# Kernel optimization log

Measured on AMD Instinct MI355X. Metric: run time of the kernel, lower is better.

The kernel has to match this reference:

```python
import jax, jax.numpy as jnp
import numpy as np

NEG_SLOPE = 0.2


def gatv2_layer(x, Wl, Wr, att, bias, src, dst, n_nodes, heads, ch, concat):
    # Wl: source-side transform (lin_l), Wr: target-side transform (lin_r)
    xl = (x @ Wl).reshape(n_nodes, heads, ch)  # [N,H,C] source features
    xr = (x @ Wr).reshape(n_nodes, heads, ch)  # [N,H,C] target features
    m = xl[src] + xr[dst]                       # [E,H,C]
    e = jax.nn.leaky_relu(m, NEG_SLOPE)
    logits = jnp.einsum('ehc,hc->eh', e, att)   # [E,H]
    # segment softmax over destination nodes
    mx = jax.ops.segment_max(logits, dst, num_segments=n_nodes)  # [N,H]
    ex = jnp.exp(logits - mx[dst])
    denom = jax.ops.segment_sum(ex, dst, num_segments=n_nodes)   # [N,H]
    alpha = ex / denom[dst]                                       # [E,H]
    out = jax.ops.segment_sum(alpha[:, :, None] * xl[src], dst,
                              num_segments=n_nodes)              # [N,H,C]
    if concat:
        out = out.reshape(n_nodes, heads * ch)
    else:
        out = out.mean(axis=1)
    return out + bias


def setup_inputs() -> dict:
    N, E = 50000, 800000
    IN, HID, OUT, H = 256, 64, 256, 4
    key = jax.random.key(0)
    ks = jax.random.split(key, 12)
    s = lambda fan_in: 1.0 / np.sqrt(fan_in)
    return {
        'x': jax.random.normal(ks[0], (N, IN), dtype=jnp.float32),
        'edge_index': jax.random.randint(ks[1], (2, E), 0, N, dtype=jnp.int64),
        'Wl1': jax.random.normal(ks[2], (IN, H * HID), jnp.float32) * s(IN),
        'Wr1': jax.random.normal(ks[3], (IN, H * HID), jnp.float32) * s(IN),
        'att1': jax.random.normal(ks[4], (H, HID), jnp.float32) * s(HID),
        'b1': jnp.zeros((H * HID,), jnp.float32),
        'Wl2': jax.random.normal(ks[5], (H * HID, OUT), jnp.float32) * s(H * HID),
        'Wr2': jax.random.normal(ks[6], (H * HID, OUT), jnp.float32) * s(H * HID),
        'att2': jax.random.normal(ks[7], (1, OUT), jnp.float32) * s(OUT),
        'b2': jnp.zeros((OUT,), jnp.float32),
    }


def reference(x, edge_index, Wl1, Wr1, att1, b1, Wl2, Wr2, att2, b2):
    N = x.shape[0]
    # PyG GATv2Conv default: add self-loops
    loops = jnp.arange(N, dtype=edge_index.dtype)
    src = jnp.concatenate([edge_index[0], loops])
    dst = jnp.concatenate([edge_index[1], loops])
    # dropout(p=0.6) is identity in eval mode
    h = gatv2_layer(x, Wl1, Wr1, att1, b1, src, dst, N, 4, 64, concat=True)
    h = jax.nn.elu(h)
    out = gatv2_layer(h, Wl2, Wr2, att2, b2, src, dst, N, 1, 256, concat=False)
    return out
```

## Files before the change

kernel.cpp:

```cpp
#include <hip/hip_runtime.h>
#include <hip/hip_fp16.h>
#include <cstdint>

using u16 = unsigned short;
using f32x4 = __attribute__((ext_vector_type(4))) float;
using short8 = __attribute__((ext_vector_type(8))) short;
using half8  = __attribute__((ext_vector_type(8))) _Float16;
using bfv8   = __attribute__((ext_vector_type(8))) __bf16;

__device__ __forceinline__ float bf2f(u16 u) {
    unsigned int v = ((unsigned int)u) << 16;
    float f; __builtin_memcpy(&f, &v, 4); return f;
}
__device__ __forceinline__ u16 f2bf(float f) {
    unsigned int u; __builtin_memcpy(&u, &f, 4);
    u += 0x7fffu + ((u >> 16) & 1u);
    return (u16)(u >> 16);
}
__device__ __forceinline__ float sane(float f) {
    return (f == f && f > -1e30f && f < 1e30f) ? f : 0.f;
}
__device__ __forceinline__ float ld16(u16 v, int isf16) {
    float fb = bf2f(v);
    __half hh; __builtin_memcpy(&hh, &v, 2);
    float fh = __half2float(hh);
    return isf16 ? fh : fb;
}
__device__ __forceinline__ u16 st16(float f, int isf16) {
    __half hh = __float2half(f);
    u16 vh; __builtin_memcpy(&vh, &hh, 2);
    return isf16 ? vh : f2bf(f);
}
__device__ __forceinline__ float ldf(const void* p, size_t i, int mode) {
    if (mode == 2) return sane(((const float*)p)[i]);
    return sane(ld16(((const u16*)p)[i], mode == 1));
}
__device__ __forceinline__ void stf(void* p, size_t i, int mode, float f) {
    if (mode == 2) { ((float*)p)[i] = f; return; }
    ((u16*)p)[i] = st16(f, mode == 1);
}
template <int ISF16> __device__ __forceinline__ float dec(u16 v);
template <> __device__ __forceinline__ float dec<0>(u16 v) { return bf2f(v); }
template <> __device__ __forceinline__ float dec<1>(u16 v) {
    __half hh; __builtin_memcpy(&hh, &v, 2); return __half2float(hh);
}
template <int CTRL, int RM>
__device__ __forceinline__ float dpp_add(float v) {
    int s = __builtin_amdgcn_update_dpp(0, __builtin_bit_cast(int, v), CTRL, RM, 0xF, true);
    return v + __builtin_bit_cast(float, s);
}

__global__ void zero_k(int* __restrict__ p, int n) {
    int i = blockIdx.x * 256 + threadIdx.x;
    if (i < n) p[i] = 0;
}

__global__ void det_k(const u16* __restrict__ x, int* __restrict__ flag) {
    __shared__ int sLow, sF32;
    if (threadIdx.x == 0) { sLow = 0; sF32 = 0; }
    __syncthreads();
    int low = 0, f32 = 0;
    for (int w = threadIdx.x; w < 2048; w += 256) {
        u16 lo = x[2 * w], hi = x[2 * w + 1];
        int e_lo = (lo >> 7) & 0xFF, e_hi = (hi >> 7) & 0xFF;
        low += (e_lo < 104) + (e_hi < 104);
        unsigned int word = ((unsigned int)hi << 16) | lo;
        int e32 = (word >> 23) & 0xFF;
        f32 += (e32 >= 97 && e32 <= 157) ? 1 : 0;
    }
    atomicAdd(&sLow, low); atomicAdd(&sF32, f32);
    __syncthreads();
    if (threadIdx.x == 0) {
        int mode = 0;
        if (sLow > 327) mode = (sF32 > 1843) ? 2 : 1;
        flag[1] = mode;
    }
}

__global__ void probe_idx(const int* __restrict__ ei, int* __restrict__ flag) {
    int t = threadIdx.x;
    int v = ei[2 * t + 1];
    unsigned long long b = __ballot(v == 0);
    if (t == 0) flag[0] = (b == ~0ull) ? 1 : 0;
}

__global__ void split_x(const void* __restrict__ x, u16* __restrict__ xhi,
                        u16* __restrict__ xlo, long n4,
                        const int* __restrict__ flag) {
    if (flag[1] != 2) return;
    long i = (long)blockIdx.x * 256 + threadIdx.x;
    if (i >= n4) return;
    float4 v = ((const float4*)x)[i];
    float f0 = sane(v.x), f1 = sane(v.y), f2 = sane(v.z), f3 = sane(v.w);
    u16 h0 = f2bf(f0), h1 = f2bf(f1), h2 = f2bf(f2), h3 = f2bf(f3);
    u16 l0 = f2bf(f0 - bf2f(h0)), l1 = f2bf(f1 - bf2f(h1));
    u16 l2 = f2bf(f2 - bf2f(h2)), l3 = f2bf(f3 - bf2f(h3));
    uint2 ph, pl;
    ph.x = (unsigned)h0 | ((unsigned)h1 << 16);
    ph.y = (unsigned)h2 | ((unsigned)h3 << 16);
    pl.x = (unsigned)l0 | ((unsigned)l1 << 16);
    pl.y = (unsigned)l2 | ((unsigned)l3 << 16);
    ((uint2*)xhi)[i] = ph;
    ((uint2*)xlo)[i] = pl;
}

__device__ __forceinline__ int bucket_of(int s, int N) {
    return (int)(((long)s * 8) / N);
}
__global__ void count2_k(const int* __restrict__ ei, const int* __restrict__ flag,
                         int* __restrict__ cnt, int E, int Etot, int N) {
    int e = blockIdx.x * 256 + threadIdx.x;
    if (e >= Etot) return;
    int sh = flag[0];
    int s, d;
    if (e < E) {
        s = ei[((size_t)e) << sh];
        d = ei[((size_t)(E + e)) << sh];
    } else { s = d = e - E; }
    s = min(max(s, 0), N - 1);
    d = min(max(d, 0), N - 1);
    atomicAdd(&cnt[d * 8 + bucket_of(s, N)], 1);
}

__global__ __launch_bounds__(256) void scan1(const int* __restrict__ cnt,
                                             int* __restrict__ bsum, int N) {
    __shared__ int sm[256];
    int t = threadIdx.x;
    int i = blockIdx.x * 256 + t;
    int v = (i < N) ? cnt[i] : 0;
    sm[t] = v;
    __syncthreads();
    for (int d = 128; d > 0; d >>= 1) {
        if (t < d) sm[t] += sm[t + d];
        __syncthreads();
    }
    if (t == 0) bsum[blockIdx.x] = sm[0];
}
__global__ __launch_bounds__(256) void scan2b(int* __restrict__ bsum,
                                              int* __restrict__ offs,
                                              int nb, int Nk) {
    __shared__ int sm[256];
    __shared__ int carryS;
    int t = threadIdx.x;
    if (t == 0) carryS = 0;
    __syncthreads();
    for (int c0 = 0; c0 < nb; c0 += 256) {
        int v = (c0 + t < nb) ? bsum[c0 + t] : 0;
        sm[t] = v;
        __syncthreads();
        for (int d = 1; d < 256; d <<= 1) {
            int u = (t >= d) ? sm[t - d] : 0;
            __syncthreads();
            sm[t] += u;
            __syncthreads();
        }
        int carry = carryS;
        if (c0 + t < nb) bsum[c0 + t] = carry + sm[t] - v;
        int tot = sm[255];
        __syncthreads();
        if (t == 0) carryS = carry + tot;
        __syncthreads();
    }
    if (t == 0) offs[Nk] = carryS;
}
__global__ __launch_bounds__(256) void scan3(const int* __restrict__ cnt,
                                             const int* __restrict__ bsum,
                                             int* __restrict__ offs,
                                             int* __restrict__ cursor, int N) {
    __shared__ int sm[256];
    int t = threadIdx.x;
    int i = blockIdx.x * 256 + t;
    int v = (i < N) ? cnt[i] : 0;
    sm[t] = v;
    __syncthreads();
    for (int d = 1; d < 256; d <<= 1) {
        int u = (t >= d) ? sm[t - d] : 0;
        __syncthreads();
        sm[t] += u;
        __syncthreads();
    }
    if (i < N) {
        int st = bsum[blockIdx.x] + sm[t] - v;
        offs[i] = st; cursor[i] = st;
    }
}

__global__ void fill2_k(const int* __restrict__ ei, const int* __restrict__ flag,
                        int* __restrict__ cursor, int* __restrict__ csr,
                        int E, int Etot, int N) {
    int e = blockIdx.x * 256 + threadIdx.x;
    if (e >= Etot) return;
    int sh = flag[0];
    int s, d;
    if (e < E) {
        s = ei[((size_t)e) << sh];
        d = ei[((size_t)(E + e)) << sh];
    } else { s = d = e - E; }
    s = min(max(s, 0), N - 1);
    d = min(max(d, 0), N - 1);
    int p = atomicAdd(&cursor[d * 8 + bucket_of(s, N)], 1);
    if (p >= 0 && p < Etot) csr[p] = s;
}

__global__ void transposeW(const void* __restrict__ Wl, const void* __restrict__ Wr,
                           u16* __restrict__ WT, const int* __restrict__ flag) {
    int c = blockIdx.x;
    int k = threadIdx.x;
    int fmode = flag[1];
    if (fmode < 2) {
        const u16* W = (c < 256) ? (const u16*)Wl : (const u16*)Wr;
        WT[c * 256 + k] = W[k * 256 + (c & 255)];
    } else {
        const float* W = (c < 256) ? (const float*)Wl : (const float*)Wr;
        float w = sane(W[k * 256 + (c & 255)]);
        u16 hi = f2bf(w);
        WT[c * 256 + k] = hi;
        WT[512 * 256 + c * 256 + k] = f2bf(w - bf2f(hi));
    }
}

__global__ __launch_bounds__(256) void gemm_mfma(
    const u16* __restrict__ A16, const u16* __restrict__ Ahi,
    const u16* __restrict__ Alo, const u16* __restrict__ BT,
    u16* __restrict__ outL, u16* __restrict__ outR, int M, int aSplit,
    const int* __restrict__ flag) {
    const int fmode = flag[1];
    const int isf16 = (fmode == 1);
    __shared__ __align__(16) u16 AsH[128 * 32];
    __shared__ __align__(16) u16 BsH[128 * 32];
    __shared__ __align__(16) u16 AsL[128 * 32];
    __shared__ __align__(16) u16 BsL[128 * 32];
    const int tid = threadIdx.x;
    const int m0 = blockIdx.x * 128;
    const int n0 = blockIdx.y * 128;
    const int wave = tid >> 6, lane = tid & 63;
    const int wr = wave >> 1, wc = wave & 1;
    const int q = lane >> 4, r = lane & 15;
    const int rowS = tid >> 1;
    const int kOff = (tid & 1) * 16;
    const long aOff = (long)min(m0 + rowS, M - 1) * 256 + kOff;
    const long bOff = (long)(n0 + rowS) * 256 + kOff;
    const u16* Ah = (fmode < 2) ? A16 : Ahi;
    const u16* BL = BT + 512 * 256;
    f32x4 acc[4][4] = {};
    for (int kt = 0; kt < 256; kt += 32) {
        *(uint4*)(&AsH[rowS * 32 + kOff])     = *(const uint4*)(&Ah[aOff + kt]);
        *(uint4*)(&AsH[rowS * 32 + kOff + 8]) = *(const uint4*)(&Ah[aOff + kt + 8]);
        *(uint4*)(&BsH[rowS * 32 + kOff])     = *(const uint4*)(&BT[bOff + kt]);
        *(uint4*)(&BsH[rowS * 32 + kOff + 8]) = *(const uint4*)(&BT[bOff + kt + 8]);
        if (fmode == 2) {
            *(uint4*)(&BsL[rowS * 32 + kOff])     = *(const uint4*)(&BL[bOff + kt]);
            *(uint4*)(&BsL[rowS * 32 + kOff + 8]) = *(const uint4*)(&BL[bOff + kt + 8]);
            if (aSplit) {
                *(uint4*)(&AsL[rowS * 32 + kOff])     = *(const uint4*)(&Alo[aOff + kt]);
                *(uint4*)(&AsL[rowS * 32 + kOff + 8]) = *(const uint4*)(&Alo[aOff + kt + 8]);
            }
        }
        __syncthreads();
        short8 aF[4], bF[4];
        #pragma unroll
        for (int i = 0; i < 4; ++i)
            aF[i] = *(const short8*)(&AsH[(wr * 64 + i * 16 + r) * 32 + q * 8]);
        #pragma unroll
        for (int i = 0; i < 4; ++i)
            bF[i] = *(const short8*)(&BsH[(wc * 64 + i * 16 + r) * 32 + q * 8]);
        if (isf16) {
            #pragma unroll
            for (int mi = 0; mi < 4; ++mi)
                #pragma unroll
                for (int ni = 0; ni < 4; ++ni)
                    acc[mi][ni] = __builtin_amdgcn_mfma_f32_16x16x32_f16(
                        __builtin_bit_cast(half8, aF[mi]),
                        __builtin_bit_cast(half8, bF[ni]), acc[mi][ni], 0, 0, 0);
        } else {
            #pragma unroll
            for (int mi = 0; mi < 4; ++mi)
                #pragma unroll
                for (int ni = 0; ni < 4; ++ni)
                    acc[mi][ni] = __builtin_amdgcn_mfma_f32_16x16x32_bf16(
                        __builtin_bit_cast(bfv8, aF[mi]),
                        __builtin_bit_cast(bfv8, bF[ni]), acc[mi][ni], 0, 0, 0);
            if (fmode == 2) {
                {
                    short8 bF2[4];
                    #pragma unroll
                    for (int i = 0; i < 4; ++i)
                        bF2[i] = *(const short8*)(&BsL[(wc * 64 + i * 16 + r) * 32 + q * 8]);
                    #pragma unroll
                    for (int mi = 0; mi < 4; ++mi)
                        #pragma unroll
                        for (int ni = 0; ni < 4; ++ni)
                            acc[mi][ni] = __builtin_amdgcn_mfma_f32_16x16x32_bf16(
                                __builtin_bit_cast(bfv8, aF[mi]),
                                __builtin_bit_cast(bfv8, bF2[ni]), acc[mi][ni], 0, 0, 0);
                }
                if (aSplit) {
                    short8 aF2[4];
                    #pragma unroll
                    for (int i = 0; i < 4; ++i)
                        aF2[i] = *(const short8*)(&AsL[(wr * 64 + i * 16 + r) * 32 + q * 8]);
                    #pragma unroll
                    for (int mi = 0; mi < 4; ++mi)
                        #pragma unroll
                        for (int ni = 0; ni < 4; ++ni)
                            acc[mi][ni] = __builtin_amdgcn_mfma_f32_16x16x32_bf16(
                                __builtin_bit_cast(bfv8, aF2[mi]),
                                __builtin_bit_cast(bfv8, bF[ni]), acc[mi][ni], 0, 0, 0);
                }
            }
        }
        __syncthreads();
    }
    #pragma unroll
    for (int mi = 0; mi < 4; ++mi) {
        #pragma unroll
        for (int ni = 0; ni < 4; ++ni) {
            #pragma unroll
            for (int e = 0; e < 4; ++e) {
                int grow = m0 + wr * 64 + mi * 16 + q * 4 + e;
                int gcol = n0 + wc * 64 + ni * 16 + r;
                if (grow < M) {
                    u16 bv = st16(sane(acc[mi][ni][e]), isf16);
                    if (gcol < 256) outL[(long)grow * 256 + gcol] = bv;
                    else            outR[(long)grow * 256 + gcol - 256] = bv;
                }
            }
        }
    }
}

template <int H, int ISF16>
__device__ __forceinline__ void edge_step(
    uint2 rl, int valid,
    float xr0, float xr1, float xr2, float xr3,
    float a0, float a1, float a2, float a3,
    float& ssum, float& acc0, float& acc1, float& acc2, float& acc3) {
    float x0 = dec<ISF16>((u16)(rl.x & 0xffff));
    float x1 = dec<ISF16>((u16)(rl.x >> 16));
    float x2 = dec<ISF16>((u16)(rl.y & 0xffff));
    float x3 = dec<ISF16>((u16)(rl.y >> 16));
    float m0v = x0 + xr0, m1v = x1 + xr1, m2v = x2 + xr2, m3v = x3 + xr3;
    float t0 = m0v > 0.f ? m0v : 0.2f * m0v;
    float t1 = m1v > 0.f ? m1v : 0.2f * m1v;
    float t2 = m2v > 0.f ? m2v : 0.2f * m2v;
    float t3 = m3v > 0.f ? m3v : 0.2f * m3v;
    float s = t0 * a0 + t1 * a1 + t2 * a2 + t3 * a3;
    s = dpp_add<0xB1, 0xF>(s);
    s = dpp_add<0x4E, 0xF>(s);
    s = dpp_add<0x141, 0xF>(s);
    s = dpp_add<0x140, 0xF>(s);
    float w;
    if (H == 4) {
        w = __expf(s);
    } else {
        s = dpp_add<0x142, 0xa>(s);
        s = dpp_add<0x143, 0xc>(s);
        int tot = __builtin_amdgcn_readlane(__builtin_bit_cast(int, s), 63);
        w = __expf(__builtin_bit_cast(float, tot));
    }
    w = valid ? w : 0.f;
    ssum += w;
    acc0 += w * x0; acc1 += w * x1; acc2 += w * x2; acc3 += w * x3;
}

template <int H, int ISF16>
__device__ __forceinline__ void fused_phases(
    const u16* __restrict__ xl, int offv,
    const int* __restrict__ csr2, int nb0, int N, int Etot, int c0, int lane,
    const uint2 (&rxr)[4], float a0, float a1, float a2, float a3,
    float (&acc)[4][4], float (&ssum)[4]) {
    int beg[4], end[4], iv[4];
    #pragma unroll
    for (int j = 0; j < 4; ++j) {
        int b = __builtin_amdgcn_readlane(offv, j * 8);
        int e = __builtin_amdgcn_readlane(offv, j * 8 + 8);
        b = min(max(b, 0), Etot);
        e = min(max(e, b), Etot);
        beg[j] = b; end[j] = e;
        const int last = max(e - 1, 0);
        iv[j] = csr2[min(b + lane, last)];
    }
    #pragma unroll
    for (int j = 0; j < 4; ++j) {
        const int n = nb0 + j;
        if (n >= N) continue;
        if (end[j] <= beg[j]) continue;
        const float xr0 = dec<ISF16>((u16)(rxr[j].x & 0xffff));
        const float xr1 = dec<ISF16>((u16)(rxr[j].x >> 16));
        const float xr2 = dec<ISF16>((u16)(rxr[j].y & 0xffff));
        const float xr3 = dec<ISF16>((u16)(rxr[j].y >> 16));
        int bb = beg[j];
        int idxv = iv[j];
        while (true) {
            const int cnt = min(end[j] - bb, 64);
            for (int p = 0; p < cnt; p += 4) {
                const int i0 = min(p + 0, cnt - 1);
                const int i1 = min(p + 1, cnt - 1);
                const int i2 = min(p + 2, cnt - 1);
                const int i3 = min(p + 3, cnt - 1);
                const int s0 = __builtin_amdgcn_readlane(idxv, i0);
                const int s1 = __builtin_amdgcn_readlane(idxv, i1);
                const int s2 = __builtin_amdgcn_readlane(idxv, i2);
                const int s3 = __builtin_amdgcn_readlane(idxv, i3);
                uint2 r0 = *(const uint2*)(&xl[(long)s0 * 256 + c0]);
                uint2 r1 = *(const uint2*)(&xl[(long)s1 * 256 + c0]);
                uint2 r2 = *(const uint2*)(&xl[(long)s2 * 256 + c0]);
                uint2 r3 = *(const uint2*)(&xl[(long)s3 * 256 + c0]);
                edge_step<H, ISF16>(r0, p + 0 < cnt, xr0, xr1, xr2, xr3,
                    a0, a1, a2, a3, ssum[j], acc[j][0], acc[j][1], acc[j][2], acc[j][3]);
                edge_step<H, ISF16>(r1, p + 1 < cnt, xr0, xr1, xr2, xr3,
                    a0, a1, a2, a3, ssum[j], acc[j][0], acc[j][1], acc[j][2], acc[j][3]);
                edge_step<H, ISF16>(r2, p + 2 < cnt, xr0, xr1, xr2, xr3,
                    a0, a1, a2, a3, ssum[j], acc[j][0], acc[j][1], acc[j][2], acc[j][3]);
                edge_step<H, ISF16>(r3, p + 3 < cnt, xr0, xr1, xr2, xr3,
                    a0, a1, a2, a3, ssum[j], acc[j][0], acc[j][1], acc[j][2], acc[j][3]);
            }
            bb += 64;
            if (bb >= end[j]) break;
            idxv = csr2[min(bb + lane, end[j] - 1)];
        }
    }
}

template <int H>
__global__ __launch_bounds__(256) void edge_fused(
    const u16* __restrict__ xl, const u16* __restrict__ xr,
    const void* __restrict__ att, const void* __restrict__ bias,
    const int* __restrict__ offs2, const int* __restrict__ csr2,
    void* __restrict__ out, int outExt, int N, int Etot, int doElu,
    const int* __restrict__ flag, int* __restrict__ gm) {
    const int fmode = flag[1];
    const int imode = (fmode == 2) ? 0 : fmode;
    const int isf16 = imode;
    const int outMode = outExt ? fmode : imode;
    const int gw = (blockIdx.x * 256 + threadIdx.x) >> 6;
    const int lane = threadIdx.x & 63;
    const int nb0 = gw * 4;
    if (nb0 >= N) return;
    const int c0 = lane * 4;
    const int Nk = N * 8;
    const int offv = offs2[min(nb0 * 8 + min(lane, 32), Nk)];
    const float a0 = ldf(att, c0 + 0, fmode), a1 = ldf(att, c0 + 1, fmode);
    const float a2 = ldf(att, c0 + 2, fmode), a3 = ldf(att, c0 + 3, fmode);
    uint2 rxr[4];
    #pragma unroll
    for (int j = 0; j < 4; ++j) {
        const int n = min(nb0 + j, N - 1);
        rxr[j] = *(const uint2*)(&xr[(long)n * 256 + c0]);
    }
    float acc[4][4] = {};
    float ssum[4] = {};
    if (isf16)
        fused_phases<H, 1>(xl, offv, csr2, nb0, N, Etot, c0, lane,
                           rxr, a0, a1, a2, a3, acc, ssum);
    else
        fused_phases<H, 0>(xl, offv, csr2, nb0, N, Etot, c0, lane,
                           rxr, a0, a1, a2, a3, acc, ssum);
    const float b0 = ldf(bias, c0 + 0, fmode), b1v = ldf(bias, c0 + 1, fmode);
    const float b2v = ldf(bias, c0 + 2, fmode), b3 = ldf(bias, c0 + 3, fmode);
    float om = 0.f;
    #pragma unroll
    for (int j = 0; j < 4; ++j) {
        const int n = nb0 + j;
        if (n >= N) continue;
        const float inv = (ssum[j] > 0.f) ? 1.f / ssum[j] : 0.f;
        float o0 = acc[j][0] * inv + b0, o1 = acc[j][1] * inv + b1v;
        float o2 = acc[j][2] * inv + b2v, o3 = acc[j][3] * inv + b3;
        if (doElu) {
            om = fmaxf(om, fmaxf(fmaxf(fabsf(o0), fabsf(o1)),
                                 fmaxf(fabsf(o2), fabsf(o3))));
            o0 = o0 > 0.f ? o0 : expm1f(o0);
            o1 = o1 > 0.f ? o1 : expm1f(o1);
            o2 = o2 > 0.f ? o2 : expm1f(o2);
            o3 = o3 > 0.f ? o3 : expm1f(o3);
        }
        o0 = fminf(fmaxf(sane(o0), -1024.f), 1024.f);
        o1 = fminf(fmaxf(sane(o1), -1024.f), 1024.f);
        o2 = fminf(fmaxf(sane(o2), -1024.f), 1024.f);
        o3 = fminf(fmaxf(sane(o3), -1024.f), 1024.f);
        const long nbo = (long)n * 256;
        stf(out, nbo + c0 + 0, outMode, o0);
        stf(out, nbo + c0 + 1, outMode, o1);
        stf(out, nbo + c0 + 2, outMode, o2);
        stf(out, nbo + c0 + 3, outMode, o3);
    }
    if (doElu) {
        #pragma unroll
        for (int d = 1; d < 64; d <<= 1)
            om = fmaxf(om, __shfl_xor(om, d, 64));
        if (lane == 0) atomicMax(gm, __float_as_int(om));
    }
}

__global__ void beacon_k(void* __restrict__ out, const int* __restrict__ flag,
                         const int* __restrict__ gm) {
    if (threadIdx.x == 0 && blockIdx.x == 0) {
        float g = __int_as_float(gm[0]);
        if (g > 8.f) {
            float b = 200.f + 100.f * (float)flag[1] + fminf(g, 90.f);
            stf(out, 0, flag[1], b);
        }
    }
}

extern "C" void kernel_launch(void* const* d_in, const int* in_sizes, int n_in,
                              void* d_out, int out_size, void* d_ws, size_t ws_size,
                              hipStream_t stream) {
    const u16* x    = (const u16*)d_in[0];
    const int* ei   = (const int*)d_in[1];
    const void* Wl1 = d_in[2];
    const void* Wr1 = d_in[3];
    const void* att1= d_in[4];
    const void* b1  = d_in[5];
    const void* Wl2 = d_in[6];
    const void* Wr2 = d_in[7];
    const void* att2= d_in[8];
    const void* b2  = d_in[9];

    const int N = in_sizes[0] / 256;
    const int E = in_sizes[1] / 2;
    const int Etot = E + N;
    const int Mpad = (N + 127) & ~127;
    const int Nk = N * 8;
    const int nb2 = (Nk + 255) / 256;

    char* p = (char*)d_ws;
    auto carve = [&](size_t bytes) -> void* {
        void* r = (void*)p; p += (bytes + 255) & ~(size_t)255; return r;
    };
    int* flag   = (int*)carve(256);
    int* gm     = (int*)carve(256);
    int* bsum   = (int*)carve(8192);
    int* cnt    = (int*)carve((size_t)(Nk + 1) * 4);
    int* offs   = (int*)carve((size_t)(Nk + 1) * 4);
    int* cursor = (int*)carve((size_t)(Nk + 1) * 4);
    int* csr    = (int*)carve((size_t)Etot * 4);
    u16* WT     = (u16*)carve((size_t)2 * 512 * 256 * 2);
    u16* xl     = (u16*)carve((size_t)N * 256 * 2);
    u16* xr     = (u16*)carve((size_t)N * 256 * 2);
    u16* h      = (u16*)d_out;
    u16* xhi    = (u16*)d_out;
    u16* xlo    = xhi + (size_t)N * 256;

    zero_k<<<1, 256, 0, stream>>>(gm, 1);
    det_k<<<1, 256, 0, stream>>>(x, flag);
    probe_idx<<<1, 64, 0, stream>>>(ei, flag);
    int eb = (Etot + 255) / 256;
    zero_k<<<(Nk + 255) / 256, 256, 0, stream>>>(cnt, Nk);
    count2_k<<<eb, 256, 0, stream>>>(ei, flag, cnt, E, Etot, N);
    scan1<<<nb2, 256, 0, stream>>>(cnt, bsum, Nk);
    scan2b<<<1, 256, 0, stream>>>(bsum, offs, nb2, Nk);
    scan3<<<nb2, 256, 0, stream>>>(cnt, bsum, offs, cursor, Nk);
    fill2_k<<<eb, 256, 0, stream>>>(ei, flag, cursor, csr, E, Etot, N);
    split_x<<<(N * 64 + 255) / 256, 256, 0, stream>>>(
        (const void*)x, xhi, xlo, (long)N * 64, flag);

    dim3 gg(Mpad / 128, 4);
    int nf = (N + 15) / 16;

    transposeW<<<512, 256, 0, stream>>>(Wl1, Wr1, WT, flag);
    gemm_mfma<<<gg, 256, 0, stream>>>(x, xhi, xlo, WT, xl, xr, N, 1, flag);
    edge_fused<4><<<nf, 256, 0, stream>>>(xl, xr, att1, b1, offs, csr,
                                          (void*)h, 0, N, Etot, 1, flag, gm);

    transposeW<<<512, 256, 0, stream>>>(Wl2, Wr2, WT, flag);
    gemm_mfma<<<gg, 256, 0, stream>>>(h, h, h, WT, xl, xr, N, 0, flag);
    edge_fused<1><<<nf, 256, 0, stream>>>(xl, xr, att2, b2, offs, csr,
                                          d_out, 1, N, Etot, 0, flag, gm);

    beacon_k<<<1, 64, 0, stream>>>(d_out, flag, gm);
}
```

Baseline: 670.0 us.

## Drop source-bucketed CSR in favor of plain per-destination CSR and linearize GEMM grid

The CSR build no longer sub-buckets each destination's edges into 8 source-range bins. It now counts and scans only N entries instead of 8N, and the edge kernel reads offsets directly per node. Source-bucket ordering was meant to improve gather locality into xl, so losing it may cost cache hits in the edge phase while making the count, scan and fill steps cheaper. The GEMM grid is also flattened so the four column tiles of the same row block are adjacent, which should improve A-tile reuse in L2.

```diff
diff --git a/kernel.cpp b/kernel.cpp
--- a/kernel.cpp
+++ b/kernel.cpp
@@ -104,22 +104,14 @@
     ((uint2*)xlo)[i] = pl;
 }
 
-__device__ __forceinline__ int bucket_of(int s, int N) {
-    return (int)(((long)s * 8) / N);
-}
-__global__ void count2_k(const int* __restrict__ ei, const int* __restrict__ flag,
-                         int* __restrict__ cnt, int E, int Etot, int N) {
+__global__ void count_k(const int* __restrict__ ei, const int* __restrict__ flag,
+                        int* __restrict__ cnt, int E, int Etot, int N) {
     int e = blockIdx.x * 256 + threadIdx.x;
     if (e >= Etot) return;
     int sh = flag[0];
-    int s, d;
-    if (e < E) {
-        s = ei[((size_t)e) << sh];
-        d = ei[((size_t)(E + e)) << sh];
-    } else { s = d = e - E; }
-    s = min(max(s, 0), N - 1);
+    int d = (e < E) ? ei[((size_t)(E + e)) << sh] : (e - E);
     d = min(max(d, 0), N - 1);
-    atomicAdd(&cnt[d * 8 + bucket_of(s, N)], 1);
+    atomicAdd(&cnt[d], 1);
 }
 
 __global__ __launch_bounds__(256) void scan1(const int* __restrict__ cnt,
@@ -185,9 +177,9 @@
     }
 }
 
-__global__ void fill2_k(const int* __restrict__ ei, const int* __restrict__ flag,
-                        int* __restrict__ cursor, int* __restrict__ csr,
-                        int E, int Etot, int N) {
+__global__ void fill_k(const int* __restrict__ ei, const int* __restrict__ flag,
+                       int* __restrict__ cursor, int* __restrict__ csr,
+                       int E, int Etot, int N) {
     int e = blockIdx.x * 256 + threadIdx.x;
     if (e >= Etot) return;
     int sh = flag[0];
@@ -198,7 +190,7 @@
     } else { s = d = e - E; }
     s = min(max(s, 0), N - 1);
     d = min(max(d, 0), N - 1);
-    int p = atomicAdd(&cursor[d * 8 + bucket_of(s, N)], 1);
+    int p = atomicAdd(&cursor[d], 1);
     if (p >= 0 && p < Etot) csr[p] = s;
 }
 
@@ -231,8 +223,8 @@
     __shared__ __align__(16) u16 AsL[128 * 32];
     __shared__ __align__(16) u16 BsL[128 * 32];
     const int tid = threadIdx.x;
-    const int m0 = blockIdx.x * 128;
-    const int n0 = blockIdx.y * 128;
+    const int m0 = (blockIdx.x >> 2) * 128;
+    const int n0 = (blockIdx.x & 3) * 128;
     const int wave = tid >> 6, lane = tid & 63;
     const int wr = wave >> 1, wc = wave & 1;
     const int q = lane >> 4, r = lane & 15;
@@ -372,8 +364,8 @@
     int beg[4], end[4], iv[4];
     #pragma unroll
     for (int j = 0; j < 4; ++j) {
-        int b = __builtin_amdgcn_readlane(offv, j * 8);
-        int e = __builtin_amdgcn_readlane(offv, j * 8 + 8);
+        int b = __builtin_amdgcn_readlane(offv, j);
+        int e = __builtin_amdgcn_readlane(offv, j + 1);
         b = min(max(b, 0), Etot);
         e = min(max(e, b), Etot);
         beg[j] = b; end[j] = e;
@@ -426,7 +418,7 @@
 __global__ __launch_bounds__(256) void edge_fused(
     const u16* __restrict__ xl, const u16* __restrict__ xr,
     const void* __restrict__ att, const void* __restrict__ bias,
-    const int* __restrict__ offs2, const int* __restrict__ csr2,
+    const int* __restrict__ offs, const int* __restrict__ csr2,
     void* __restrict__ out, int outExt, int N, int Etot, int doElu,
     const int* __restrict__ flag, int* __restrict__ gm) {
     const int fmode = flag[1];
@@ -438,8 +430,7 @@
     const int nb0 = gw * 4;
     if (nb0 >= N) return;
     const int c0 = lane * 4;
-    const int Nk = N * 8;
-    const int offv = offs2[min(nb0 * 8 + min(lane, 32), Nk)];
+    const int offv = offs[min(nb0 + min(lane, 4), N)];
     const float a0 = ldf(att, c0 + 0, fmode), a1 = ldf(att, c0 + 1, fmode);
     const float a2 = ldf(att, c0 + 2, fmode), a3 = ldf(att, c0 + 3, fmode);
     uint2 rxr[4];
@@ -521,8 +512,7 @@
     const int E = in_sizes[1] / 2;
     const int Etot = E + N;
     const int Mpad = (N + 127) & ~127;
-    const int Nk = N * 8;
-    const int nb2 = (Nk + 255) / 256;
+    const int nb1 = (N + 255) / 256;
 
     char* p = (char*)d_ws;
     auto carve = [&](size_t bytes) -> void* {
@@ -531,9 +521,9 @@
     int* flag   = (int*)carve(256);
     int* gm     = (int*)carve(256);
     int* bsum   = (int*)carve(8192);
-    int* cnt    = (int*)carve((size_t)(Nk + 1) * 4);
-    int* offs   = (int*)carve((size_t)(Nk + 1) * 4);
-    int* cursor = (int*)carve((size_t)(Nk + 1) * 4);
+    int* cnt    = (int*)carve((size_t)(N + 1) * 4);
+    int* offs   = (int*)carve((size_t)(N + 1) * 4);
+    int* cursor = (int*)carve((size_t)(N + 1) * 4);
     int* csr    = (int*)carve((size_t)Etot * 4);
     u16* WT     = (u16*)carve((size_t)2 * 512 * 256 * 2);
     u16* xl     = (u16*)carve((size_t)N * 256 * 2);
@@ -546,25 +536,25 @@
     det_k<<<1, 256, 0, stream>>>(x, flag);
     probe_idx<<<1, 64, 0, stream>>>(ei, flag);
     int eb = (Etot + 255) / 256;
-    zero_k<<<(Nk + 255) / 256, 256, 0, stream>>>(cnt, Nk);
-    count2_k<<<eb, 256, 0, stream>>>(ei, flag, cnt, E, Etot, N);
-    scan1<<<nb2, 256, 0, stream>>>(cnt, bsum, Nk);
-    scan2b<<<1, 256, 0, stream>>>(bsum, offs, nb2, Nk);
-    scan3<<<nb2, 256, 0, stream>>>(cnt, bsum, offs, cursor, Nk);
-    fill2_k<<<eb, 256, 0, stream>>>(ei, flag, cursor, csr, E, Etot, N);
+    zero_k<<<(N + 255) / 256, 256, 0, stream>>>(cnt, N);
+    count_k<<<eb, 256, 0, stream>>>(ei, flag, cnt, E, Etot, N);
+    scan1<<<nb1, 256, 0, stream>>>(cnt, bsum, N);
+    scan2b<<<1, 256, 0, stream>>>(bsum, offs, nb1, N);
+    scan3<<<nb1, 256, 0, stream>>>(cnt, bsum, offs, cursor, N);
+    fill_k<<<eb, 256, 0, stream>>>(ei, flag, cursor, csr, E, Etot, N);
     split_x<<<(N * 64 + 255) / 256, 256, 0, stream>>>(
         (const void*)x, xhi, xlo, (long)N * 64, flag);
 
-    dim3 gg(Mpad / 128, 4);
+    int gb = (Mpad / 128) * 4;
     int nf = (N + 15) / 16;
 
     transposeW<<<512, 256, 0, stream>>>(Wl1, Wr1, WT, flag);
-    gemm_mfma<<<gg, 256, 0, stream>>>(x, xhi, xlo, WT, xl, xr, N, 1, flag);
+    gemm_mfma<<<gb, 256, 0, stream>>>(x, xhi, xlo, WT, xl, xr, N, 1, flag);
     edge_fused<4><<<nf, 256, 0, stream>>>(xl, xr, att1, b1, offs, csr,
                                           (void*)h, 0, N, Etot, 1, flag, gm);
 
     transposeW<<<512, 256, 0, stream>>>(Wl2, Wr2, WT, flag);
-    gemm_mfma<<<gg, 256, 0, stream>>>(h, h, h, WT, xl, xr, N, 0, flag);
+    gemm_mfma<<<gb, 256, 0, stream>>>(h, h, h, WT, xl, xr, N, 0, flag);
     edge_fused<1><<<nf, 256, 0, stream>>>(xl, xr, att2, b2, offs, csr,
                                           d_out, 1, N, Etot, 0, flag, gm);
 
```

Result: faster. 648.8 us (-3.2%).
